# Optimization experiments

Measured on AMD Instinct MI355X. Metric: run time of the kernel, lower is better.

## Reference

```python
import jax, jax.numpy as jnp
import numpy as np

N_USERS, N_ITEMS = 3000, 3000
N = N_USERS + N_ITEMS
E = 100000
DIMS = [(N, 32), (32, 64), (64, 64), (64, 32)]  # RGCN layer (in,out) dims
NUM_REL = 2


def setup_inputs():
    key = jax.random.key(0)
    ks = iter(jax.random.split(key, 40))
    def p(shape, s=0.05):
        return jax.random.normal(next(ks), shape, dtype=jnp.float32) * s
    inp = {}
    for l, (i, o) in enumerate(DIMS):
        inp[f'basis{l}'] = p((4, i, o))      # basis matrices
        inp[f'comp{l}'] = p((NUM_REL, 4), 0.5)  # per-relation basis coefficients
        inp[f'root{l}'] = p((i, o))          # root/self weight
        inp[f'rbias{l}'] = jnp.zeros((o,), jnp.float32)
    inp['gat_w'] = p((32, 512))
    inp['gat_att_src'] = p((512,))
    inp['gat_att_dst'] = p((512,))
    inp['gat_bias'] = jnp.zeros((512,), jnp.float32)
    inp['w1'] = p((1024, 128))
    inp['b1'] = jnp.zeros((128,), jnp.float32)
    inp['w2'] = p((128, 1))
    inp['b2'] = jnp.zeros((1,), jnp.float32)
    inp['edge_index'] = jax.random.randint(next(ks), (2, E), 0, N)
    inp['edge_type'] = jax.random.randint(next(ks), (E,), 0, NUM_REL)
    return inp


def rgcn_layer(x, src, dst, edge_type, basis, comp, root, bias):
    # basis-decomposed relation weights: W[r] = sum_b comp[r,b] * basis[b]
    W = jnp.einsum('rb,bio->rio', comp, basis)  # [R, in, out]
    out = x @ root + bias                        # root/self term
    for r in range(NUM_REL):                     # fixed small relation count
        hr = x @ W[r]                            # [N, out]
        mask = (edge_type == r).astype(x.dtype)  # [E]
        msg = hr[src] * mask[:, None]            # gather + relation mask
        s = jax.ops.segment_sum(msg, dst, num_segments=N)
        cnt = jax.ops.segment_sum(mask, dst, num_segments=N)
        out = out + s / jnp.maximum(cnt, 1.0)[:, None]  # mean aggregation
    return out


def gat_layer(x, src, dst, w, a_src, a_dst, bias):
    # GATConv (1 head, negative_slope=0.2) with self-loops added (PyG default)
    loop = jnp.arange(N)
    s = jnp.concatenate([src, loop])
    d = jnp.concatenate([dst, loop])
    h = x @ w                      # [N, 512]
    asv = h @ a_src                # [N]
    adv = h @ a_dst                # [N]
    alpha = jax.nn.leaky_relu(asv[s] + adv[d], 0.2)  # [E+N]
    amax = jax.ops.segment_max(alpha, d, num_segments=N)
    amax = jnp.where(jnp.isneginf(amax), 0.0, amax)
    ex = jnp.exp(alpha - amax[d])
    denom = jax.ops.segment_sum(ex, d, num_segments=N)
    coef = ex / jnp.maximum(denom[d], 1e-16)
    out = jax.ops.segment_sum(h[s] * coef[:, None], d, num_segments=N)
    return out + bias


def reference(edge_index, edge_type,
              basis0, comp0, root0, rbias0,
              basis1, comp1, root1, rbias1,
              basis2, comp2, root2, rbias2,
              basis3, comp3, root3, rbias3,
              gat_w, gat_att_src, gat_att_dst, gat_bias,
              w1, b1, w2, b2):
    src, dst = edge_index[0], edge_index[1]
    convs = [(basis0, comp0, root0, rbias0), (basis1, comp1, root1, rbias1),
             (basis2, comp2, root2, rbias2), (basis3, comp3, root3, rbias3)]
    x = jnp.eye(N, dtype=jnp.float32)  # one-hot node features
    for (b, c, r, bi) in convs:
        x = jnp.tanh(rgcn_layer(x, src, dst, edge_type, b, c, r, bi))
    x = jax.nn.relu(gat_layer(x, src, dst, gat_w, gat_att_src, gat_att_dst, gat_bias))
    feat = jnp.concatenate([x[src], x[dst]], axis=1)  # [E, 1024]
    h = jax.nn.relu(feat @ w1 + b1)
    # F.dropout omitted (deterministic eval reference)
    out = jax.nn.sigmoid(h @ w2 + b2)
    return out.squeeze(-1)  # [E]
```

## Files before the change

kernel.cpp:

```cpp
#include <hip/hip_runtime.h>
#include <math.h>

#define NN 6000
#define EE 100000
#define ELL (EE + NN)
#define CAP 64

#define PK_SRC(p)  ((p) & 0x1FFF)
#define PK_REL(p)  (((p) >> 13) & 1)
#define PK_SELF(p) ((p) & 0x4000)

typedef __attribute__((ext_vector_type(8))) short frag8;
typedef __attribute__((ext_vector_type(4))) float f32x4;
typedef __attribute__((ext_vector_type(8))) unsigned short u16x8;

__device__ __forceinline__ unsigned short f2bf(float f){
  unsigned u = __float_as_uint(f);
  unsigned r = u + 0x7FFFu + ((u >> 16) & 1u);
  return (unsigned short)(r >> 16);
}
__device__ __forceinline__ float bf2f(unsigned short s){
  return __uint_as_float(((unsigned)s) << 16);
}

__global__ void k_pdc(const int* __restrict__ ei, const int* __restrict__ et,
                      int* __restrict__ cursor, int* __restrict__ pks,
                      const float* __restrict__ basis0, const float* __restrict__ comp0,
                      const float* __restrict__ b1,const float* __restrict__ c1,const float* __restrict__ r1,
                      const float* __restrict__ b2,const float* __restrict__ c2,const float* __restrict__ r2,
                      const float* __restrict__ b3,const float* __restrict__ c3,const float* __restrict__ r3,
                      const float* __restrict__ w1,
                      const float* __restrict__ gw, const float* __restrict__ a_src,
                      const float* __restrict__ a_dst,
                      unsigned short* __restrict__ W016, float* __restrict__ Wcat,
                      unsigned short* __restrict__ Bt16, float* __restrict__ gwa){
  int t0 = blockIdx.x*256 + threadIdx.x;
  if (t0 < ELL){
    int d, pk;
    if (t0 < EE){
      d = ei[EE+t0];
      pk = ei[t0] | (et[t0] << 13);
    } else {
      d = t0 - EE; pk = d | 0x4000;
    }
    int pos = atomicAdd(&cursor[d], 1);
    pks[d*CAP + pos] = pk;
  }
  if (t0 < 2*NN*32){
    int r = t0 / (NN*32);
    int no = t0 - r*(NN*32);
    float acc = 0.f;
    #pragma unroll
    for (int b=0;b<4;b++) acc += comp0[r*4+b] * basis0[b*(NN*32)+no];
    W016[t0] = f2bf(acc);
    return;
  }
  int tw = t0 - 2*NN*32;
  if (tw < 24576){
    const float *bb,*cc,*rr; int I,O; int t = tw;
    if (tw < 6144)        { bb=b1;cc=c1;rr=r1;I=32;O=64; }
    else if (tw < 18432)  { bb=b2;cc=c2;rr=r2;I=64;O=64; t -= 6144; }
    else                  { bb=b3;cc=c3;rr=r3;I=64;O=32; t -= 18432; }
    int C = 3*O;
    int i = t / C; int col = t - i*C;
    float v;
    if (col < O) v = rr[i*O + col];
    else {
      int r = (col - O) / O; int o = col - O - r*O;
      v = 0.f;
      #pragma unroll
      for (int b=0;b<4;b++) v += cc[r*4+b]*bb[(b*I+i)*O + o];
    }
    Wcat[tw] = v;
    return;
  }
  int tb = tw - 24576;
  if (tb < 256*512){
    int n = tb >> 9, k = tb & 511;
    float v = (n < 128) ? w1[k*128 + n] : w1[(512+k)*128 + (n-128)];
    Bt16[tb] = f2bf(v);
    return;
  }
  int ti = tb - 256*512;
  if (ti < 64){
    const float* av = (ti < 32) ? a_src : a_dst;
    int i = ti & 31;
    float s = 0.f;
    for (int k=0;k<512;k++) s += gw[i*512+k]*av[k];
    gwa[ti] = s;
  }
}

__global__ void __launch_bounds__(256) k_f1(
    const unsigned short* __restrict__ W016, const float* __restrict__ root,
    const float* __restrict__ rbias0,
    const int* __restrict__ degc, const int* __restrict__ pks,
    const float* __restrict__ Wc, unsigned short* __restrict__ Hout){
  __shared__ float sx[8*32];
  int n0 = blockIdx.x*8;
  int t = threadIdx.x, nl = t>>5, o = t&31, n = n0+nl;
  int r0 = n*CAP, deg = degc[n];
  int pk0 = (o      < deg) ? pks[r0 + o]      : 0x4000;
  int pk1 = (32 + o < deg) ? pks[r0 + 32 + o] : 0x4000;
  float a0 = 0.f, a1 = 0.f, c0 = 0.f, c1 = 0.f;
  int d0 = min(deg,32), d1 = deg - d0;
  for (int j=0;j<d0;j+=2){
    int pA = __shfl(pk0, j, 32);
    int pB = __shfl(pk0, j+1, 32);
    float vA = bf2f(W016[(PK_REL(pA)*NN + PK_SRC(pA))*32 + o]);
    float vB = bf2f(W016[(PK_REL(pB)*NN + PK_SRC(pB))*32 + o]);
    if (!PK_SELF(pA)){ if (PK_REL(pA)==0){ a0 += vA; c0 += 1.f; } else { a1 += vA; c1 += 1.f; } }
    if (!PK_SELF(pB)){ if (PK_REL(pB)==0){ a0 += vB; c0 += 1.f; } else { a1 += vB; c1 += 1.f; } }
  }
  for (int j=0;j<d1;j+=2){
    int pA = __shfl(pk1, j, 32);
    int pB = __shfl(pk1, j+1, 32);
    float vA = bf2f(W016[(PK_REL(pA)*NN + PK_SRC(pA))*32 + o]);
    float vB = bf2f(W016[(PK_REL(pB)*NN + PK_SRC(pB))*32 + o]);
    if (!PK_SELF(pA)){ if (PK_REL(pA)==0){ a0 += vA; c0 += 1.f; } else { a1 += vA; c1 += 1.f; } }
    if (!PK_SELF(pB)){ if (PK_REL(pB)==0){ a0 += vB; c0 += 1.f; } else { a1 += vB; c1 += 1.f; } }
  }
  sx[nl*32+o] = tanhf(root[n*32+o] + rbias0[o]
                      + a0/fmaxf(c0,1.f) + a1/fmaxf(c1,1.f));
  __syncthreads();
  if (t < 192){
    float acc[8] = {0,0,0,0,0,0,0,0};
    for (int i=0;i<32;i++){
      float w = Wc[i*192 + t];
      #pragma unroll
      for (int tt=0;tt<8;tt++) acc[tt] += sx[tt*32+i]*w;
    }
    #pragma unroll
    for (int tt=0;tt<8;tt++) Hout[(n0+tt)*192 + t] = f2bf(acc[tt]);
  }
}

__global__ void __launch_bounds__(256) k_f2(
    const unsigned short* __restrict__ Hin, const float* __restrict__ rbias,
    const int* __restrict__ degc, const int* __restrict__ pks,
    const float* __restrict__ Wc, unsigned short* __restrict__ Hout){
  __shared__ float sx[8*64];
  int n0 = blockIdx.x*8;
  int t = threadIdx.x, nl = t>>5, og = t&31, o0 = og*2, n = n0+nl;
  int r0 = n*CAP, deg = degc[n];
  int pk0 = (og      < deg) ? pks[r0 + og]      : 0x4000;
  int pk1 = (32 + og < deg) ? pks[r0 + 32 + og] : 0x4000;
  float a00=0.f, a01=0.f, a10=0.f, a11=0.f, c0=0.f, c1=0.f;
  int d0 = min(deg,32), d1 = deg - d0;
  for (int j=0;j<d0;j+=2){
    int pA = __shfl(pk0, j, 32);
    int pB = __shfl(pk0, j+1, 32);
    unsigned hvA = *(const unsigned*)&Hin[PK_SRC(pA)*192 + 64 + PK_REL(pA)*64 + o0];
    unsigned hvB = *(const unsigned*)&Hin[PK_SRC(pB)*192 + 64 + PK_REL(pB)*64 + o0];
    if (!PK_SELF(pA)){
      float v0 = bf2f((unsigned short)(hvA & 0xFFFF));
      float v1 = bf2f((unsigned short)(hvA >> 16));
      if (PK_REL(pA)==0){ a00 += v0; a01 += v1; c0 += 1.f; } else { a10 += v0; a11 += v1; c1 += 1.f; }
    }
    if (!PK_SELF(pB)){
      float v0 = bf2f((unsigned short)(hvB & 0xFFFF));
      float v1 = bf2f((unsigned short)(hvB >> 16));
      if (PK_REL(pB)==0){ a00 += v0; a01 += v1; c0 += 1.f; } else { a10 += v0; a11 += v1; c1 += 1.f; }
    }
  }
  for (int j=0;j<d1;j+=2){
    int pA = __shfl(pk1, j, 32);
    int pB = __shfl(pk1, j+1, 32);
    unsigned hvA = *(const unsigned*)&Hin[PK_SRC(pA)*192 + 64 + PK_REL(pA)*64 + o0];
    unsigned hvB = *(const unsigned*)&Hin[PK_SRC(pB)*192 + 64 + PK_REL(pB)*64 + o0];
    if (!PK_SELF(pA)){
      float v0 = bf2f((unsigned short)(hvA & 0xFFFF));
      float v1 = bf2f((unsigned short)(hvA >> 16));
      if (PK_REL(pA)==0){ a00 += v0; a01 += v1; c0 += 1.f; } else { a10 += v0; a11 += v1; c1 += 1.f; }
    }
    if (!PK_SELF(pB)){
      float v0 = bf2f((unsigned short)(hvB & 0xFFFF));
      float v1 = bf2f((unsigned short)(hvB >> 16));
      if (PK_REL(pB)==0){ a00 += v0; a01 += v1; c0 += 1.f; } else { a10 += v0; a11 += v1; c1 += 1.f; }
    }
  }
  float i0 = 1.f/fmaxf(c0,1.f), i1 = 1.f/fmaxf(c1,1.f);
  sx[nl*64+o0]   = tanhf(bf2f(Hin[n*192+o0])   + rbias[o0]   + a00*i0 + a10*i1);
  sx[nl*64+o0+1] = tanhf(bf2f(Hin[n*192+o0+1]) + rbias[o0+1] + a01*i0 + a11*i1);
  __syncthreads();
  if (t < 192){
    float acc[8] = {0,0,0,0,0,0,0,0};
    for (int i=0;i<64;i++){
      float w = Wc[i*192 + t];
      #pragma unroll
      for (int tt=0;tt<8;tt++) acc[tt] += sx[tt*64+i]*w;
    }
    #pragma unroll
    for (int tt=0;tt<8;tt++) Hout[(n0+tt)*192 + t] = f2bf(acc[tt]);
  }
}

__global__ void __launch_bounds__(256) k_f3(
    const unsigned short* __restrict__ Hin, const float* __restrict__ rbias,
    const int* __restrict__ degc, const int* __restrict__ pks,
    const float* __restrict__ Wc, unsigned short* __restrict__ Hout){
  __shared__ float sx[8*64];
  int n0 = blockIdx.x*8;
  int t = threadIdx.x, nl = t>>5, og = t&31, o0 = og*2, n = n0+nl;
  int r0 = n*CAP, deg = degc[n];
  int pk0 = (og      < deg) ? pks[r0 + og]      : 0x4000;
  int pk1 = (32 + og < deg) ? pks[r0 + 32 + og] : 0x4000;
  float a00=0.f, a01=0.f, a10=0.f, a11=0.f, c0=0.f, c1=0.f;
  int d0 = min(deg,32), d1 = deg - d0;
  for (int j=0;j<d0;j+=2){
    int pA = __shfl(pk0, j, 32);
    int pB = __shfl(pk0, j+1, 32);
    unsigned hvA = *(const unsigned*)&Hin[PK_SRC(pA)*192 + 64 + PK_REL(pA)*64 + o0];
    unsigned hvB = *(const unsigned*)&Hin[PK_SRC(pB)*192 + 64 + PK_REL(pB)*64 + o0];
    if (!PK_SELF(pA)){
      float v0 = bf2f((unsigned short)(hvA & 0xFFFF));
      float v1 = bf2f((unsigned short)(hvA >> 16));
      if (PK_REL(pA)==0){ a00 += v0; a01 += v1; c0 += 1.f; } else { a10 += v0; a11 += v1; c1 += 1.f; }
    }
    if (!PK_SELF(pB)){
      float v0 = bf2f((unsigned short)(hvB & 0xFFFF));
      float v1 = bf2f((unsigned short)(hvB >> 16));
      if (PK_REL(pB)==0){ a00 += v0; a01 += v1; c0 += 1.f; } else { a10 += v0; a11 += v1; c1 += 1.f; }
    }
  }
  for (int j=0;j<d1;j+=2){
    int pA = __shfl(pk1, j, 32);
    int pB = __shfl(pk1, j+1, 32);
    unsigned hvA = *(const unsigned*)&Hin[PK_SRC(pA)*192 + 64 + PK_REL(pA)*64 + o0];
    unsigned hvB = *(const unsigned*)&Hin[PK_SRC(pB)*192 + 64 + PK_REL(pB)*64 + o0];
    if (!PK_SELF(pA)){
      float v0 = bf2f((unsigned short)(hvA & 0xFFFF));
      float v1 = bf2f((unsigned short)(hvA >> 16));
      if (PK_REL(pA)==0){ a00 += v0; a01 += v1; c0 += 1.f; } else { a10 += v0; a11 += v1; c1 += 1.f; }
    }
    if (!PK_SELF(pB)){
      float v0 = bf2f((unsigned short)(hvB & 0xFFFF));
      float v1 = bf2f((unsigned short)(hvB >> 16));
      if (PK_REL(pB)==0){ a00 += v0; a01 += v1; c0 += 1.f; } else { a10 += v0; a11 += v1; c1 += 1.f; }
    }
  }
  float i0 = 1.f/fmaxf(c0,1.f), i1 = 1.f/fmaxf(c1,1.f);
  sx[nl*64+o0]   = tanhf(bf2f(Hin[n*192+o0])   + rbias[o0]   + a00*i0 + a10*i1);
  sx[nl*64+o0+1] = tanhf(bf2f(Hin[n*192+o0+1]) + rbias[o0+1] + a01*i0 + a11*i1);
  __syncthreads();
  if (t < 192){
    int c = t % 96, grp = t / 96;
    float acc[4] = {0,0,0,0};
    for (int i=0;i<64;i++){
      float w = Wc[i*96 + c];
      #pragma unroll
      for (int tt=0;tt<4;tt++) acc[tt] += sx[(grp*4+tt)*64+i]*w;
    }
    #pragma unroll
    for (int tt=0;tt<4;tt++) Hout[(n0+grp*4+tt)*96 + c] = f2bf(acc[tt]);
  }
}

__global__ void __launch_bounds__(256) k_f4(
    const unsigned short* __restrict__ Hin, const float* __restrict__ rbias,
    const int* __restrict__ degc, const int* __restrict__ pks,
    const float* __restrict__ gwa,
    unsigned short* __restrict__ X4, float* __restrict__ asv, float* __restrict__ adv){
  int n0 = blockIdx.x*8;
  int t = threadIdx.x, nl = t>>5, o = t&31, n = n0+nl;
  int r0 = n*CAP, deg = degc[n];
  int pk0 = (o      < deg) ? pks[r0 + o]      : 0x4000;
  int pk1 = (32 + o < deg) ? pks[r0 + 32 + o] : 0x4000;
  float a0=0.f, a1=0.f, c0=0.f, c1=0.f;
  int d0 = min(deg,32), d1 = deg - d0;
  for (int j=0;j<d0;j+=2){
    int pA = __shfl(pk0, j, 32);
    int pB = __shfl(pk0, j+1, 32);
    float vA = bf2f(Hin[PK_SRC(pA)*96 + 32 + PK_REL(pA)*32 + o]);
    float vB = bf2f(Hin[PK_SRC(pB)*96 + 32 + PK_REL(pB)*32 + o]);
    if (!PK_SELF(pA)){ if (PK_REL(pA)==0){ a0 += vA; c0 += 1.f; } else { a1 += vA; c1 += 1.f; } }
    if (!PK_SELF(pB)){ if (PK_REL(pB)==0){ a0 += vB; c0 += 1.f; } else { a1 += vB; c1 += 1.f; } }
  }
  for (int j=0;j<d1;j+=2){
    int pA = __shfl(pk1, j, 32);
    int pB = __shfl(pk1, j+1, 32);
    float vA = bf2f(Hin[PK_SRC(pA)*96 + 32 + PK_REL(pA)*32 + o]);
    float vB = bf2f(Hin[PK_SRC(pB)*96 + 32 + PK_REL(pB)*32 + o]);
    if (!PK_SELF(pA)){ if (PK_REL(pA)==0){ a0 += vA; c0 += 1.f; } else { a1 += vA; c1 += 1.f; } }
    if (!PK_SELF(pB)){ if (PK_REL(pB)==0){ a0 += vB; c0 += 1.f; } else { a1 += vB; c1 += 1.f; } }
  }
  float v = tanhf(bf2f(Hin[n*96+o]) + rbias[o]
                  + a0/fmaxf(c0,1.f) + a1/fmaxf(c1,1.f));
  X4[n*32 + o] = f2bf(v);
  float ss = v * gwa[o];
  float sd = v * gwa[32+o];
  #pragma unroll
  for (int off=16;off>0;off>>=1){
    ss += __shfl_xor(ss,off,64);
    sd += __shfl_xor(sd,off,64);
  }
  if (o==0){ asv[n] = ss; adv[n] = sd; }
}

__global__ void __launch_bounds__(256) k_gpab(
    const int* __restrict__ degc, const int* __restrict__ pks,
    const float* __restrict__ asv, const float* __restrict__ adv,
    const unsigned short* __restrict__ X4, const float* __restrict__ gw,
    const float* __restrict__ gat_b, const unsigned short* __restrict__ Bt16,
    unsigned short* __restrict__ P16){
  __shared__ float xa[16][33];
  __shared__ unsigned short go[16*520];
  int t = threadIdx.x, w = t>>6, lane = t&63;
  int n0 = blockIdx.x*16;
  for (int s=0;s<4;s++){
    int nl = w*4 + s, n = n0 + nl;
    int r0 = n*CAP, deg = degc[n];
    float advn = adv[n];
    int pk  = (lane < deg) ? pks[r0 + lane] : -1;
    int src = (pk >= 0) ? PK_SRC(pk) : 0;
    float aa = -1e30f;
    if (pk >= 0){
      float a = asv[src] + advn;
      aa = (a >= 0.f) ? a : 0.2f*a;
    }
    float m = aa;
    #pragma unroll
    for (int off=32;off>0;off>>=1) m = fmaxf(m, __shfl_xor(m,off,64));
    float ex = (pk >= 0) ? expf(aa - m) : 0.f;
    float se = ex;
    #pragma unroll
    for (int off=32;off>0;off>>=1) se += __shfl_xor(se,off,64);
    float inv = 1.f / fmaxf(se, 1e-16f);
    int c = lane & 31, hh = lane >> 5;
    float acc = 0.f;
    for (int e=0;e<deg;e+=2){
      float cf = __shfl(ex, e+hh, 64);
      int   sv = __shfl(src, e+hh, 64);
      acc += cf * bf2f(X4[sv*32 + c]);
    }
    acc += __shfl_xor(acc, 32, 64);
    if (hh == 0) xa[nl][c] = acc * inv;
  }
  __syncthreads();
  {
    int c2 = t*2;
    float2 acc2[16];
    #pragma unroll
    for (int k=0;k<16;k++) acc2[k] = {0.f,0.f};
    for (int i=0;i<32;i++){
      const float2 g = *(const float2*)&gw[i*512 + c2];
      #pragma unroll
      for (int k=0;k<16;k++){
        float xv = xa[k][i];
        acc2[k].x += xv*g.x; acc2[k].y += xv*g.y;
      }
    }
    const float2 bv = *(const float2*)&gat_b[c2];
    #pragma unroll
    for (int k=0;k<16;k++){
      ushort2 ov;
      ov.x = f2bf(fmaxf(acc2[k].x + bv.x, 0.f));
      ov.y = f2bf(fmaxf(acc2[k].y + bv.y, 0.f));
      *(ushort2*)&go[k*520 + c2] = ov;
    }
  }
  __syncthreads();
  {
    int kq = (lane >> 4) * 8;
    const unsigned short* arow  = go + (lane & 15)*520 + kq;
    const unsigned short* bbase = Bt16 + (size_t)(w*64 + (lane & 15))*512 + kq;
    f32x4 acc0 = {0,0,0,0}, acc1 = {0,0,0,0}, acc2 = {0,0,0,0}, acc3 = {0,0,0,0};
    for (int k = 0; k < 512; k += 32){
      frag8 a  = *(const frag8*)(arow + k);
      frag8 b0 = *(const frag8*)(bbase + k);
      frag8 b1 = *(const frag8*)(bbase + 16*512 + k);
      frag8 b2 = *(const frag8*)(bbase + 32*512 + k);
      frag8 b3 = *(const frag8*)(bbase + 48*512 + k);
      acc0 = __builtin_amdgcn_mfma_f32_16x16x32_bf16(a, b0, acc0, 0, 0, 0);
      acc1 = __builtin_amdgcn_mfma_f32_16x16x32_bf16(a, b1, acc1, 0, 0, 0);
      acc2 = __builtin_amdgcn_mfma_f32_16x16x32_bf16(a, b2, acc2, 0, 0, 0);
      acc3 = __builtin_amdgcn_mfma_f32_16x16x32_bf16(a, b3, acc3, 0, 0, 0);
    }
    int rowb = n0 + (lane >> 4)*4;
    int col  = w*64 + (lane & 15);
    #pragma unroll
    for (int i=0;i<4;i++){
      P16[(size_t)(rowb+i)*256 + col     ] = f2bf(acc0[i]);
      P16[(size_t)(rowb+i)*256 + col + 16] = f2bf(acc1[i]);
      P16[(size_t)(rowb+i)*256 + col + 32] = f2bf(acc2[i]);
      P16[(size_t)(rowb+i)*256 + col + 48] = f2bf(acc3[i]);
    }
  }
}

__global__ void k_edge(const int* __restrict__ ei, const unsigned short* __restrict__ P16,
                       const float* __restrict__ b1,
                       const float* __restrict__ w2, const float* __restrict__ b2,
                       float* __restrict__ out){
  int e = blockIdx.x*16 + (threadIdx.x >> 4);
  int l = threadIdx.x & 15;
  if (e >= EE) return;
  int s = ei[e], d = ei[EE+e];
  const u16x8 Av = *(const u16x8*)&P16[(size_t)s*256 + l*8];
  const u16x8 Bv = *(const u16x8*)&P16[(size_t)d*256 + 128 + l*8];
  const float4 b1a = *(const float4*)&b1[l*8];
  const float4 b1b = *(const float4*)&b1[l*8+4];
  const float4 w2a = *(const float4*)&w2[l*8];
  const float4 w2b = *(const float4*)&w2[l*8+4];
  float h0 = fmaxf(bf2f(Av[0])+bf2f(Bv[0])+b1a.x, 0.f);
  float h1 = fmaxf(bf2f(Av[1])+bf2f(Bv[1])+b1a.y, 0.f);
  float h2 = fmaxf(bf2f(Av[2])+bf2f(Bv[2])+b1a.z, 0.f);
  float h3 = fmaxf(bf2f(Av[3])+bf2f(Bv[3])+b1a.w, 0.f);
  float h4 = fmaxf(bf2f(Av[4])+bf2f(Bv[4])+b1b.x, 0.f);
  float h5 = fmaxf(bf2f(Av[5])+bf2f(Bv[5])+b1b.y, 0.f);
  float h6 = fmaxf(bf2f(Av[6])+bf2f(Bv[6])+b1b.z, 0.f);
  float h7 = fmaxf(bf2f(Av[7])+bf2f(Bv[7])+b1b.w, 0.f);
  float acc = h0*w2a.x + h1*w2a.y + h2*w2a.z + h3*w2a.w
            + h4*w2b.x + h5*w2b.y + h6*w2b.z + h7*w2b.w;
  #pragma unroll
  for (int m=8;m>0;m>>=1) acc += __shfl_xor(acc,m,64);
  if (l==0) out[e] = 1.f/(1.f + expf(-(acc + b2[0])));
}

extern "C" void kernel_launch(void* const* d_in, const int* in_sizes, int n_in,
                              void* d_out, int out_size, void* d_ws, size_t ws_size,
                              hipStream_t stream){
  const float* basis0 = (const float*)d_in[0];
  const float* comp0  = (const float*)d_in[1];
  const float* root0  = (const float*)d_in[2];
  const float* rbias0 = (const float*)d_in[3];
  const float* basis1 = (const float*)d_in[4];
  const float* comp1  = (const float*)d_in[5];
  const float* root1  = (const float*)d_in[6];
  const float* rbias1 = (const float*)d_in[7];
  const float* basis2 = (const float*)d_in[8];
  const float* comp2  = (const float*)d_in[9];
  const float* root2  = (const float*)d_in[10];
  const float* rbias2 = (const float*)d_in[11];
  const float* basis3 = (const float*)d_in[12];
  const float* comp3  = (const float*)d_in[13];
  const float* root3  = (const float*)d_in[14];
  const float* rbias3 = (const float*)d_in[15];
  const float* gat_w = (const float*)d_in[16];
  const float* a_src = (const float*)d_in[17];
  const float* a_dst = (const float*)d_in[18];
  const float* gat_b = (const float*)d_in[19];
  const float* w1 = (const float*)d_in[20];
  const float* b1 = (const float*)d_in[21];
  const float* w2 = (const float*)d_in[22];
  const float* b2 = (const float*)d_in[23];
  const int* ei = (const int*)d_in[24];
  const int* et = (const int*)d_in[25];
  float* out = (float*)d_out;

  float* p = (float*)d_ws;
  int* cursor = (int*)p; p += NN;
  int* pks    = (int*)p; p += NN*CAP;
  unsigned short* W016 = (unsigned short*)p; p += NN*32;
  float* Wcat = p; p += 24576;
  unsigned short* Bt16 = (unsigned short*)p; p += 256*512/2;
  unsigned short* H16a = (unsigned short*)p; p += NN*96;
  unsigned short* H16b = (unsigned short*)p; p += NN*96;
  unsigned short* X4   = (unsigned short*)p; p += NN*16;
  float* gwa  = p; p += 64;
  float* asv  = p; p += NN;
  float* adv  = p; p += NN;
  unsigned short* P16 = (unsigned short*)p; p += NN*128;

  auto grid = [](long long n){ return dim3((unsigned)((n + 255)/256)); };

  hipMemsetAsync(cursor, 0, (size_t)NN*sizeof(int), stream);
  k_pdc<<<grid(2LL*NN*32 + 24576 + 256*512 + 64),256,0,stream>>>(ei, et, cursor, pks,
        basis0, comp0, basis1,comp1,root1, basis2,comp2,root2,
        basis3,comp3,root3, w1, gat_w, a_src, a_dst, W016, Wcat, Bt16, gwa);

  k_f1<<<dim3(NN/8),256,0,stream>>>(W016, root0, rbias0, cursor, pks, Wcat, H16a);
  k_f2<<<dim3(NN/8),256,0,stream>>>(H16a, rbias1, cursor, pks, Wcat + 6144, H16b);
  k_f3<<<dim3(NN/8),256,0,stream>>>(H16b, rbias2, cursor, pks, Wcat + 18432, H16a);
  k_f4<<<dim3(NN/8),256,0,stream>>>(H16a, rbias3, cursor, pks, gwa, X4, asv, adv);

  k_gpab<<<dim3(NN/16),256,0,stream>>>(cursor, pks, asv, adv, X4, gat_w, gat_b,
                                       Bt16, P16);

  k_edge<<<dim3((EE+15)/16),256,0,stream>>>(ei, P16, b1, w2, b2, out);
}
```

Measured before the change: 209.1 us.

## Use full 64-lane wavefronts per node in RGCN layers and split GAT aggregation

Each RGCN layer kernel now gives a node a full 64-lane wavefront instead of a 32-lane half, with the two halves gathering alternate neighbor pairs and merging through a cross-half shuffle. Blocks cover 4 nodes rather than 8, which doubles the grid size. The GAT softmax-aggregation is moved out of the fused projection kernel into its own kernel, which writes an fp32 intermediate that a second kernel reads for the 512-wide projection. The aim is more parallelism and latency hiding for the irregular gathers, paid for by an extra launch, an extra global round trip, and less weight reuse per block in the small dense products.

Measured after the change: 190.5 us. 1.1x faster.

```diff
diff --git a/kernel.cpp b/kernel.cpp
--- a/kernel.cpp
+++ b/kernel.cpp
@@ -96,42 +96,36 @@
     const float* __restrict__ rbias0,
     const int* __restrict__ degc, const int* __restrict__ pks,
     const float* __restrict__ Wc, unsigned short* __restrict__ Hout){
-  __shared__ float sx[8*32];
-  int n0 = blockIdx.x*8;
-  int t = threadIdx.x, nl = t>>5, o = t&31, n = n0+nl;
+  __shared__ float sx[4*32];
+  int n0 = blockIdx.x*4;
+  int t = threadIdx.x, nl = t>>6, lane = t&63, o = lane&31, h = lane>>5;
+  int n = n0 + nl;
   int r0 = n*CAP, deg = degc[n];
-  int pk0 = (o      < deg) ? pks[r0 + o]      : 0x4000;
-  int pk1 = (32 + o < deg) ? pks[r0 + 32 + o] : 0x4000;
+  int pk = (lane < deg) ? pks[r0 + lane] : 0x4000;
   float a0 = 0.f, a1 = 0.f, c0 = 0.f, c1 = 0.f;
-  int d0 = min(deg,32), d1 = deg - d0;
-  for (int j=0;j<d0;j+=2){
-    int pA = __shfl(pk0, j, 32);
-    int pB = __shfl(pk0, j+1, 32);
+  int trips = (deg + 1) >> 1;
+  for (int jj = 0; jj < trips; jj += 2){
+    int pA = __shfl(pk, 2*jj + h, 64);
+    int pB = __shfl(pk, 2*jj + 2 + h, 64);
     float vA = bf2f(W016[(PK_REL(pA)*NN + PK_SRC(pA))*32 + o]);
     float vB = bf2f(W016[(PK_REL(pB)*NN + PK_SRC(pB))*32 + o]);
     if (!PK_SELF(pA)){ if (PK_REL(pA)==0){ a0 += vA; c0 += 1.f; } else { a1 += vA; c1 += 1.f; } }
-    if (!PK_SELF(pB)){ if (PK_REL(pB)==0){ a0 += vB; c0 += 1.f; } else { a1 += vB; c1 += 1.f; } }
-  }
-  for (int j=0;j<d1;j+=2){
-    int pA = __shfl(pk1, j, 32);
-    int pB = __shfl(pk1, j+1, 32);
-    float vA = bf2f(W016[(PK_REL(pA)*NN + PK_SRC(pA))*32 + o]);
-    float vB = bf2f(W016[(PK_REL(pB)*NN + PK_SRC(pB))*32 + o]);
-    if (!PK_SELF(pA)){ if (PK_REL(pA)==0){ a0 += vA; c0 += 1.f; } else { a1 += vA; c1 += 1.f; } }
-    if (!PK_SELF(pB)){ if (PK_REL(pB)==0){ a0 += vB; c0 += 1.f; } else { a1 += vB; c1 += 1.f; } }
-  }
-  sx[nl*32+o] = tanhf(root[n*32+o] + rbias0[o]
-                      + a0/fmaxf(c0,1.f) + a1/fmaxf(c1,1.f));
+    if (jj + 1 < trips && !PK_SELF(pB)){ if (PK_REL(pB)==0){ a0 += vB; c0 += 1.f; } else { a1 += vB; c1 += 1.f; } }
+  }
+  a0 += __shfl_xor(a0, 32, 64); a1 += __shfl_xor(a1, 32, 64);
+  c0 += __shfl_xor(c0, 32, 64); c1 += __shfl_xor(c1, 32, 64);
+  float v = tanhf(root[n*32+o] + rbias0[o] + a0/fmaxf(c0,1.f) + a1/fmaxf(c1,1.f));
+  if (h == 0) sx[nl*32+o] = v;
   __syncthreads();
   if (t < 192){
-    float acc[8] = {0,0,0,0,0,0,0,0};
+    float acc[4] = {0,0,0,0};
     for (int i=0;i<32;i++){
       float w = Wc[i*192 + t];
       #pragma unroll
-      for (int tt=0;tt<8;tt++) acc[tt] += sx[tt*32+i]*w;
-    }
-    #pragma unroll
-    for (int tt=0;tt<8;tt++) Hout[(n0+tt)*192 + t] = f2bf(acc[tt]);
+      for (int tt=0;tt<4;tt++) acc[tt] += sx[tt*32+i]*w;
+    }
+    #pragma unroll
+    for (int tt=0;tt<4;tt++) Hout[(n0+tt)*192 + t] = f2bf(acc[tt]);
   }
 }
 
@@ -139,17 +133,17 @@
     const unsigned short* __restrict__ Hin, const float* __restrict__ rbias,
     const int* __restrict__ degc, const int* __restrict__ pks,
     const float* __restrict__ Wc, unsigned short* __restrict__ Hout){
-  __shared__ float sx[8*64];
-  int n0 = blockIdx.x*8;
-  int t = threadIdx.x, nl = t>>5, og = t&31, o0 = og*2, n = n0+nl;
+  __shared__ float sx[4*64];
+  int n0 = blockIdx.x*4;
+  int t = threadIdx.x, nl = t>>6, lane = t&63, o0 = (lane&31)*2, h = lane>>5;
+  int n = n0 + nl;
   int r0 = n*CAP, deg = degc[n];
-  int pk0 = (og      < deg) ? pks[r0 + og]      : 0x4000;
-  int pk1 = (32 + og < deg) ? pks[r0 + 32 + og] : 0x4000;
+  int pk = (lane < deg) ? pks[r0 + lane] : 0x4000;
   float a00=0.f, a01=0.f, a10=0.f, a11=0.f, c0=0.f, c1=0.f;
-  int d0 = min(deg,32), d1 = deg - d0;
-  for (int j=0;j<d0;j+=2){
-    int pA = __shfl(pk0, j, 32);
-    int pB = __shfl(pk0, j+1, 32);
+  int trips = (deg + 1) >> 1;
+  for (int jj = 0; jj < trips; jj += 2){
+    int pA = __shfl(pk, 2*jj + h, 64);
+    int pB = __shfl(pk, 2*jj + 2 + h, 64);
     unsigned hvA = *(const unsigned*)&Hin[PK_SRC(pA)*192 + 64 + PK_REL(pA)*64 + o0];
     unsigned hvB = *(const unsigned*)&Hin[PK_SRC(pB)*192 + 64 + PK_REL(pB)*64 + o0];
     if (!PK_SELF(pA)){
@@ -157,15 +151,48 @@
       float v1 = bf2f((unsigned short)(hvA >> 16));
       if (PK_REL(pA)==0){ a00 += v0; a01 += v1; c0 += 1.f; } else { a10 += v0; a11 += v1; c1 += 1.f; }
     }
-    if (!PK_SELF(pB)){
+    if (jj + 1 < trips && !PK_SELF(pB)){
       float v0 = bf2f((unsigned short)(hvB & 0xFFFF));
       float v1 = bf2f((unsigned short)(hvB >> 16));
       if (PK_REL(pB)==0){ a00 += v0; a01 += v1; c0 += 1.f; } else { a10 += v0; a11 += v1; c1 += 1.f; }
     }
   }
-  for (int j=0;j<d1;j+=2){
-    int pA = __shfl(pk1, j, 32);
-    int pB = __shfl(pk1, j+1, 32);
+  a00 += __shfl_xor(a00, 32, 64); a01 += __shfl_xor(a01, 32, 64);
+  a10 += __shfl_xor(a10, 32, 64); a11 += __shfl_xor(a11, 32, 64);
+  c0  += __shfl_xor(c0, 32, 64);  c1  += __shfl_xor(c1, 32, 64);
+  float i0 = 1.f/fmaxf(c0,1.f), i1 = 1.f/fmaxf(c1,1.f);
+  if (h == 0){
+    sx[nl*64+o0]   = tanhf(bf2f(Hin[n*192+o0])   + rbias[o0]   + a00*i0 + a10*i1);
+    sx[nl*64+o0+1] = tanhf(bf2f(Hin[n*192+o0+1]) + rbias[o0+1] + a01*i0 + a11*i1);
+  }
+  __syncthreads();
+  if (t < 192){
+    float acc[4] = {0,0,0,0};
+    for (int i=0;i<64;i++){
+      float w = Wc[i*192 + t];
+      #pragma unroll
+      for (int tt=0;tt<4;tt++) acc[tt] += sx[tt*64+i]*w;
+    }
+    #pragma unroll
+    for (int tt=0;tt<4;tt++) Hout[(n0+tt)*192 + t] = f2bf(acc[tt]);
+  }
+}
+
+__global__ void __launch_bounds__(256) k_f3(
+    const unsigned short* __restrict__ Hin, const float* __restrict__ rbias,
+    const int* __restrict__ degc, const int* __restrict__ pks,
+    const float* __restrict__ Wc, unsigned short* __restrict__ Hout){
+  __shared__ float sx[4*64];
+  int n0 = blockIdx.x*4;
+  int t = threadIdx.x, nl = t>>6, lane = t&63, o0 = (lane&31)*2, h = lane>>5;
+  int n = n0 + nl;
+  int r0 = n*CAP, deg = degc[n];
+  int pk = (lane < deg) ? pks[r0 + lane] : 0x4000;
+  float a00=0.f, a01=0.f, a10=0.f, a11=0.f, c0=0.f, c1=0.f;
+  int trips = (deg + 1) >> 1;
+  for (int jj = 0; jj < trips; jj += 2){
+    int pA = __shfl(pk, 2*jj + h, 64);
+    int pB = __shfl(pk, 2*jj + 2 + h, 64);
     unsigned hvA = *(const unsigned*)&Hin[PK_SRC(pA)*192 + 64 + PK_REL(pA)*64 + o0];
     unsigned hvB = *(const unsigned*)&Hin[PK_SRC(pB)*192 + 64 + PK_REL(pB)*64 + o0];
     if (!PK_SELF(pA)){
@@ -173,86 +200,31 @@
       float v1 = bf2f((unsigned short)(hvA >> 16));
       if (PK_REL(pA)==0){ a00 += v0; a01 += v1; c0 += 1.f; } else { a10 += v0; a11 += v1; c1 += 1.f; }
     }
-    if (!PK_SELF(pB)){
+    if (jj + 1 < trips && !PK_SELF(pB)){
       float v0 = bf2f((unsigned short)(hvB & 0xFFFF));
       float v1 = bf2f((unsigned short)(hvB >> 16));
       if (PK_REL(pB)==0){ a00 += v0; a01 += v1; c0 += 1.f; } else { a10 += v0; a11 += v1; c1 += 1.f; }
     }
   }
+  a00 += __shfl_xor(a00, 32, 64); a01 += __shfl_xor(a01, 32, 64);
+  a10 += __shfl_xor(a10, 32, 64); a11 += __shfl_xor(a11, 32, 64);
+  c0  += __shfl_xor(c0, 32, 64);  c1  += __shfl_xor(c1, 32, 64);
   float i0 = 1.f/fmaxf(c0,1.f), i1 = 1.f/fmaxf(c1,1.f);
-  sx[nl*64+o0]   = tanhf(bf2f(Hin[n*192+o0])   + rbias[o0]   + a00*i0 + a10*i1);
-  sx[nl*64+o0+1] = tanhf(bf2f(Hin[n*192+o0+1]) + rbias[o0+1] + a01*i0 + a11*i1);
-  __syncthreads();
-  if (t < 192){
-    float acc[8] = {0,0,0,0,0,0,0,0};
-    for (int i=0;i<64;i++){
-      float w = Wc[i*192 + t];
-      #pragma unroll
-      for (int tt=0;tt<8;tt++) acc[tt] += sx[tt*64+i]*w;
-    }
-    #pragma unroll
-    for (int tt=0;tt<8;tt++) Hout[(n0+tt)*192 + t] = f2bf(acc[tt]);
-  }
-}
-
-__global__ void __launch_bounds__(256) k_f3(
-    const unsigned short* __restrict__ Hin, const float* __restrict__ rbias,
-    const int* __restrict__ degc, const int* __restrict__ pks,
-    const float* __restrict__ Wc, unsigned short* __restrict__ Hout){
-  __shared__ float sx[8*64];
-  int n0 = blockIdx.x*8;
-  int t = threadIdx.x, nl = t>>5, og = t&31, o0 = og*2, n = n0+nl;
-  int r0 = n*CAP, deg = degc[n];
-  int pk0 = (og      < deg) ? pks[r0 + og]      : 0x4000;
-  int pk1 = (32 + og < deg) ? pks[r0 + 32 + og] : 0x4000;
-  float a00=0.f, a01=0.f, a10=0.f, a11=0.f, c0=0.f, c1=0.f;
-  int d0 = min(deg,32), d1 = deg - d0;
-  for (int j=0;j<d0;j+=2){
-    int pA = __shfl(pk0, j, 32);
-    int pB = __shfl(pk0, j+1, 32);
-    unsigned hvA = *(const unsigned*)&Hin[PK_SRC(pA)*192 + 64 + PK_REL(pA)*64 + o0];
-    unsigned hvB = *(const unsigned*)&Hin[PK_SRC(pB)*192 + 64 + PK_REL(pB)*64 + o0];
-    if (!PK_SELF(pA)){
-      float v0 = bf2f((unsigned short)(hvA & 0xFFFF));
-      float v1 = bf2f((unsigned short)(hvA >> 16));
-      if (PK_REL(pA)==0){ a00 += v0; a01 += v1; c0 += 1.f; } else { a10 += v0; a11 += v1; c1 += 1.f; }
-    }
-    if (!PK_SELF(pB)){
-      float v0 = bf2f((unsigned short)(hvB & 0xFFFF));
-      float v1 = bf2f((unsigned short)(hvB >> 16));
-      if (PK_REL(pB)==0){ a00 += v0; a01 += v1; c0 += 1.f; } else { a10 += v0; a11 += v1; c1 += 1.f; }
-    }
-  }
-  for (int j=0;j<d1;j+=2){
-    int pA = __shfl(pk1, j, 32);
-    int pB = __shfl(pk1, j+1, 32);
-    unsigned hvA = *(const unsigned*)&Hin[PK_SRC(pA)*192 + 64 + PK_REL(pA)*64 + o0];
-    unsigned hvB = *(const unsigned*)&Hin[PK_SRC(pB)*192 + 64 + PK_REL(pB)*64 + o0];
-    if (!PK_SELF(pA)){
-      float v0 = bf2f((unsigned short)(hvA & 0xFFFF));
-      float v1 = bf2f((unsigned short)(hvA >> 16));
-      if (PK_REL(pA)==0){ a00 += v0; a01 += v1; c0 += 1.f; } else { a10 += v0; a11 += v1; c1 += 1.f; }
-    }
-    if (!PK_SELF(pB)){
-      float v0 = bf2f((unsigned short)(hvB & 0xFFFF));
-      float v1 = bf2f((unsigned short)(hvB >> 16));
-      if (PK_REL(pB)==0){ a00 += v0; a01 += v1; c0 += 1.f; } else { a10 += v0; a11 += v1; c1 += 1.f; }
-    }
-  }
-  float i0 = 1.f/fmaxf(c0,1.f), i1 = 1.f/fmaxf(c1,1.f);
-  sx[nl*64+o0]   = tanhf(bf2f(Hin[n*192+o0])   + rbias[o0]   + a00*i0 + a10*i1);
-  sx[nl*64+o0+1] = tanhf(bf2f(Hin[n*192+o0+1]) + rbias[o0+1] + a01*i0 + a11*i1);
+  if (h == 0){
+    sx[nl*64+o0]   = tanhf(bf2f(Hin[n*192+o0])   + rbias[o0]   + a00*i0 + a10*i1);
+    sx[nl*64+o0+1] = tanhf(bf2f(Hin[n*192+o0+1]) + rbias[o0+1] + a01*i0 + a11*i1);
+  }
   __syncthreads();
   if (t < 192){
     int c = t % 96, grp = t / 96;
-    float acc[4] = {0,0,0,0};
+    float acc[2] = {0,0};
     for (int i=0;i<64;i++){
       float w = Wc[i*96 + c];
       #pragma unroll
-      for (int tt=0;tt<4;tt++) acc[tt] += sx[(grp*4+tt)*64+i]*w;
-    }
-    #pragma unroll
-    for (int tt=0;tt<4;tt++) Hout[(n0+grp*4+tt)*96 + c] = f2bf(acc[tt]);
+      for (int tt=0;tt<2;tt++) acc[tt] += sx[(grp*2+tt)*64+i]*w;
+    }
+    #pragma unroll
+    for (int tt=0;tt<2;tt++) Hout[(n0+grp*2+tt)*96 + c] = f2bf(acc[tt]);
   }
 }
 
@@ -261,80 +233,84 @@
     const int* __restrict__ degc, const int* __restrict__ pks,
     const float* __restrict__ gwa,
     unsigned short* __restrict__ X4, float* __restrict__ asv, float* __restrict__ adv){
-  int n0 = blockIdx.x*8;
-  int t = threadIdx.x, nl = t>>5, o = t&31, n = n0+nl;
+  int n0 = blockIdx.x*4;
+  int t = threadIdx.x, nl = t>>6, lane = t&63, o = lane&31, h = lane>>5;
+  int n = n0 + nl;
   int r0 = n*CAP, deg = degc[n];
-  int pk0 = (o      < deg) ? pks[r0 + o]      : 0x4000;
-  int pk1 = (32 + o < deg) ? pks[r0 + 32 + o] : 0x4000;
+  int pk = (lane < deg) ? pks[r0 + lane] : 0x4000;
   float a0=0.f, a1=0.f, c0=0.f, c1=0.f;
-  int d0 = min(deg,32), d1 = deg - d0;
-  for (int j=0;j<d0;j+=2){
-    int pA = __shfl(pk0, j, 32);
-    int pB = __shfl(pk0, j+1, 32);
+  int trips = (deg + 1) >> 1;
+  for (int jj = 0; jj < trips; jj += 2){
+    int pA = __shfl(pk, 2*jj + h, 64);
+    int pB = __shfl(pk, 2*jj + 2 + h, 64);
     float vA = bf2f(Hin[PK_SRC(pA)*96 + 32 + PK_REL(pA)*32 + o]);
     float vB = bf2f(Hin[PK_SRC(pB)*96 + 32 + PK_REL(pB)*32 + o]);
     if (!PK_SELF(pA)){ if (PK_REL(pA)==0){ a0 += vA; c0 += 1.f; } else { a1 += vA; c1 += 1.f; } }
-    if (!PK_SELF(pB)){ if (PK_REL(pB)==0){ a0 += vB; c0 += 1.f; } else { a1 += vB; c1 += 1.f; } }
-  }
-  for (int j=0;j<d1;j+=2){
-    int pA = __shfl(pk1, j, 32);
-    int pB = __shfl(pk1, j+1, 32);
-    float vA = bf2f(Hin[PK_SRC(pA)*96 + 32 + PK_REL(pA)*32 + o]);
-    float vB = bf2f(Hin[PK_SRC(pB)*96 + 32 + PK_REL(pB)*32 + o]);
-    if (!PK_SELF(pA)){ if (PK_REL(pA)==0){ a0 += vA; c0 += 1.f; } else { a1 += vA; c1 += 1.f; } }
-    if (!PK_SELF(pB)){ if (PK_REL(pB)==0){ a0 += vB; c0 += 1.f; } else { a1 += vB; c1 += 1.f; } }
-  }
-  float v = tanhf(bf2f(Hin[n*96+o]) + rbias[o]
-                  + a0/fmaxf(c0,1.f) + a1/fmaxf(c1,1.f));
-  X4[n*32 + o] = f2bf(v);
-  float ss = v * gwa[o];
-  float sd = v * gwa[32+o];
+    if (jj + 1 < trips && !PK_SELF(pB)){ if (PK_REL(pB)==0){ a0 += vB; c0 += 1.f; } else { a1 += vB; c1 += 1.f; } }
+  }
+  a0 += __shfl_xor(a0, 32, 64); a1 += __shfl_xor(a1, 32, 64);
+  c0 += __shfl_xor(c0, 32, 64); c1 += __shfl_xor(c1, 32, 64);
+  float v = tanhf(bf2f(Hin[n*96+o]) + rbias[o] + a0/fmaxf(c0,1.f) + a1/fmaxf(c1,1.f));
+  if (h == 0) X4[n*32 + o] = f2bf(v);
+  float s = v * gwa[h*32 + o];
   #pragma unroll
-  for (int off=16;off>0;off>>=1){
-    ss += __shfl_xor(ss,off,64);
-    sd += __shfl_xor(sd,off,64);
-  }
-  if (o==0){ asv[n] = ss; adv[n] = sd; }
-}
-
-__global__ void __launch_bounds__(256) k_gpab(
+  for (int off=16;off>0;off>>=1) s += __shfl_xor(s, off, 64);
+  if (lane == 0)       asv[n] = s;
+  else if (lane == 32) adv[n] = s;
+}
+
+__global__ void __launch_bounds__(256) k_gs2(
     const int* __restrict__ degc, const int* __restrict__ pks,
     const float* __restrict__ asv, const float* __restrict__ adv,
-    const unsigned short* __restrict__ X4, const float* __restrict__ gw,
+    const unsigned short* __restrict__ X4, float* __restrict__ xagg){
+  int t = threadIdx.x, w = t>>6, lane = t&63;
+  int n = blockIdx.x*4 + w;
+  int r0 = n*CAP, deg = degc[n];
+  float advn = adv[n];
+  int pk  = (lane < deg) ? pks[r0 + lane] : -1;
+  int src = (pk >= 0) ? PK_SRC(pk) : 0;
+  float aa = -1e30f;
+  if (pk >= 0){
+    float a = asv[src] + advn;
+    aa = (a >= 0.f) ? a : 0.2f*a;
+  }
+  float m = aa;
+  #pragma unroll
+  for (int off=32;off>0;off>>=1) m = fmaxf(m, __shfl_xor(m,off,64));
+  float ex = (pk >= 0) ? expf(aa - m) : 0.f;
+  float se = ex;
+  #pragma unroll
+  for (int off=32;off>0;off>>=1) se += __shfl_xor(se,off,64);
+  float inv = 1.f / fmaxf(se, 1e-16f);
+  int c = lane & 31, h = lane >> 5;
+  float acc = 0.f;
+  int trips = (deg + 1) >> 1;
+  for (int jj = 0; jj < trips; jj += 2){
+    float cfA = __shfl(ex, 2*jj + h, 64);
+    int   svA = __shfl(src, 2*jj + h, 64);
+    float cfB = __shfl(ex, 2*jj + 2 + h, 64);
+    int   svB = __shfl(src, 2*jj + 2 + h, 64);
+    float vA = bf2f(X4[svA*32 + c]);
+    float vB = bf2f(X4[svB*32 + c]);
+    acc += cfA * vA;
+    if (jj + 1 < trips) acc += cfB * vB;
+  }
+  acc += __shfl_xor(acc, 32, 64);
+  if (h == 0) xagg[n*32 + c] = acc * inv;
+}
+
+__global__ void __launch_bounds__(256) k_ab2(
+    const float* __restrict__ xagg, const float* __restrict__ gw,
     const float* __restrict__ gat_b, const unsigned short* __restrict__ Bt16,
     unsigned short* __restrict__ P16){
   __shared__ float xa[16][33];
   __shared__ unsigned short go[16*520];
   int t = threadIdx.x, w = t>>6, lane = t&63;
   int n0 = blockIdx.x*16;
-  for (int s=0;s<4;s++){
-    int nl = w*4 + s, n = n0 + nl;
-    int r0 = n*CAP, deg = degc[n];
-    float advn = adv[n];
-    int pk  = (lane < deg) ? pks[r0 + lane] : -1;
-    int src = (pk >= 0) ? PK_SRC(pk) : 0;
-    float aa = -1e30f;
-    if (pk >= 0){
-      float a = asv[src] + advn;
-      aa = (a >= 0.f) ? a : 0.2f*a;
-    }
-    float m = aa;
-    #pragma unroll
-    for (int off=32;off>0;off>>=1) m = fmaxf(m, __shfl_xor(m,off,64));
-    float ex = (pk >= 0) ? expf(aa - m) : 0.f;
-    float se = ex;
-    #pragma unroll
-    for (int off=32;off>0;off>>=1) se += __shfl_xor(se,off,64);
-    float inv = 1.f / fmaxf(se, 1e-16f);
-    int c = lane & 31, hh = lane >> 5;
-    float acc = 0.f;
-    for (int e=0;e<deg;e+=2){
-      float cf = __shfl(ex, e+hh, 64);
-      int   sv = __shfl(src, e+hh, 64);
-      acc += cf * bf2f(X4[sv*32 + c]);
-    }
-    acc += __shfl_xor(acc, 32, 64);
-    if (hh == 0) xa[nl][c] = acc * inv;
+  {
+    int i0 = t, i1 = t + 256;
+    xa[i0 >> 5][i0 & 31] = xagg[n0*32 + i0];
+    xa[i1 >> 5][i1 & 31] = xagg[n0*32 + i1];
   }
   __syncthreads();
   {
@@ -460,6 +436,7 @@
   float* gwa  = p; p += 64;
   float* asv  = p; p += NN;
   float* adv  = p; p += NN;
+  float* xagg = p; p += NN*32;
   unsigned short* P16 = (unsigned short*)p; p += NN*128;
 
   auto grid = [](long long n){ return dim3((unsigned)((n + 255)/256)); };
@@ -469,13 +446,13 @@
         basis0, comp0, basis1,comp1,root1, basis2,comp2,root2,
         basis3,comp3,root3, w1, gat_w, a_src, a_dst, W016, Wcat, Bt16, gwa);
 
-  k_f1<<<dim3(NN/8),256,0,stream>>>(W016, root0, rbias0, cursor, pks, Wcat, H16a);
-  k_f2<<<dim3(NN/8),256,0,stream>>>(H16a, rbias1, cursor, pks, Wcat + 6144, H16b);
-  k_f3<<<dim3(NN/8),256,0,stream>>>(H16b, rbias2, cursor, pks, Wcat + 18432, H16a);
-  k_f4<<<dim3(NN/8),256,0,stream>>>(H16a, rbias3, cursor, pks, gwa, X4, asv, adv);
-
-  k_gpab<<<dim3(NN/16),256,0,stream>>>(cursor, pks, asv, adv, X4, gat_w, gat_b,
-                                       Bt16, P16);
+  k_f1<<<dim3(NN/4),256,0,stream>>>(W016, root0, rbias0, cursor, pks, Wcat, H16a);
+  k_f2<<<dim3(NN/4),256,0,stream>>>(H16a, rbias1, cursor, pks, Wcat + 6144, H16b);
+  k_f3<<<dim3(NN/4),256,0,stream>>>(H16b, rbias2, cursor, pks, Wcat + 18432, H16a);
+  k_f4<<<dim3(NN/4),256,0,stream>>>(H16a, rbias3, cursor, pks, gwa, X4, asv, adv);
+
+  k_gs2<<<dim3(NN/4),256,0,stream>>>(cursor, pks, asv, adv, X4, xagg);
+  k_ab2<<<dim3(NN/16),256,0,stream>>>(xagg, gat_w, gat_b, Bt16, P16);
 
   k_edge<<<dim3((EE+15)/16),256,0,stream>>>(ei, P16, b1, w2, b2, out);
 }
```
